# Performance work log

Measured on AMD Instinct MI355X. Metric: run time of the kernel, lower is better.

Reference implementation:

```python
import jax, jax.numpy as jnp
import numpy as np

N = 100000
E = 1600000
C_IN = 128
C_HID = 128


def setup_inputs() -> dict:
    key = jax.random.key(0)
    ks = jax.random.split(key, 6)
    x = jax.random.normal(ks[0], (N, C_IN), dtype=jnp.float32)
    edge_index = jax.random.randint(ks[1], (2, E), 0, N, dtype=jnp.int64)
    # GCNConv params: linear weight + bias per layer (glorot-ish scale)
    W1 = jax.random.normal(ks[2], (C_IN, C_HID), dtype=jnp.float32) / np.sqrt(C_IN)
    b1 = jnp.zeros((C_HID,), dtype=jnp.float32)
    W2 = jax.random.normal(ks[3], (C_HID, C_HID), dtype=jnp.float32) / np.sqrt(C_HID)
    b2 = jnp.zeros((C_HID,), dtype=jnp.float32)
    return {"x": x, "edge_index": edge_index, "W1": W1, "b1": b1, "W2": W2, "b2": b2}


def _gcn_conv(x, W, b, src, dst, n_nodes):
    # PyG GCNConv: h = D^{-1/2} (A + I) D^{-1/2} (x W) + b
    h = x @ W  # [N, C_out]
    # add self-loops
    loop = jnp.arange(n_nodes, dtype=src.dtype)
    s = jnp.concatenate([src, loop])
    d = jnp.concatenate([dst, loop])
    ones = jnp.ones(s.shape[0], dtype=h.dtype)
    deg = jax.ops.segment_sum(ones, d, num_segments=n_nodes)  # in-degree incl self-loop
    dinv = jnp.where(deg > 0, jax.lax.rsqrt(deg), 0.0)
    norm = dinv[s] * dinv[d]  # [E+N]
    msg = h[s] * norm[:, None]  # gather + scale
    out = jax.ops.segment_sum(msg, d, num_segments=n_nodes)  # scatter-add
    return out + b


def reference(x, edge_index, W1, b1, W2, b2):
    src, dst = edge_index[0], edge_index[1]
    h = jax.nn.relu(_gcn_conv(x, W1, b1, src, dst, N))
    h = jax.nn.relu(_gcn_conv(h, W2, b2, src, dst, N))
    return h
```

## Files before the change

kernel.cpp:

```cpp
#include <hip/hip_runtime.h>
#include <hip/hip_bf16.h>

#define GCN_N 100000
#define GB1 1563

typedef unsigned short u16;
typedef unsigned int u32;
typedef float f32x4 __attribute__((ext_vector_type(4)));
typedef short bf16x8 __attribute__((ext_vector_type(8)));

union v16 { uint4 u; bf16x8 h; };

__device__ inline u16 f2bf(float f) {
    u32 u = __float_as_uint(f);
    return (u16)((u + 0x7fffu + ((u >> 16) & 1u)) >> 16);
}
__device__ inline u32 pack2(float a, float b) {
    return (u32)f2bf(a) | ((u32)f2bf(b) << 16);
}
__device__ inline float bf_lo(u32 u) { return __uint_as_float(u << 16); }
__device__ inline float bf_hi(u32 u) { return __uint_as_float(u & 0xffff0000u); }

__device__ inline void addu8(float* a, float4 v) {
    u32 u;
    u = __float_as_uint(v.x); a[0] += bf_lo(u); a[1] += bf_hi(u);
    u = __float_as_uint(v.y); a[2] += bf_lo(u); a[3] += bf_hi(u);
    u = __float_as_uint(v.z); a[4] += bf_lo(u); a[5] += bf_hi(u);
    u = __float_as_uint(v.w); a[6] += bf_lo(u); a[7] += bf_hi(u);
}
__device__ inline void setu8(float* a, float4 v) {
    u32 u;
    u = __float_as_uint(v.x); a[0] = bf_lo(u); a[1] = bf_hi(u);
    u = __float_as_uint(v.y); a[2] = bf_lo(u); a[3] = bf_hi(u);
    u = __float_as_uint(v.z); a[4] = bf_lo(u); a[5] = bf_hi(u);
    u = __float_as_uint(v.w); a[6] = bf_lo(u); a[7] = bf_hi(u);
}

__device__ inline void mfma16(f32x4& d, uint4 a, uint4 b) {
    v16 av, bv; av.u = a; bv.u = b;
    d = __builtin_amdgcn_mfma_f32_16x16x32_bf16(av.h, bv.h, d, 0, 0, 0);
}


__global__ __launch_bounds__(256) void k_rank(const int* __restrict__ dst,
                                              int* __restrict__ cnt,
                                              int* __restrict__ rank, int E) {
    int i = blockIdx.x * 256 + threadIdx.x;
    if (i < E) rank[i] = atomicAdd(&cnt[dst[i]], 1);
}

__global__ __launch_bounds__(256) void k_bsum(const int* __restrict__ cnt,
                                              int* __restrict__ bsum, int n) {
    int i = blockIdx.x * 256 + threadIdx.x;
    int v = (i < n) ? cnt[i] : 0;
    #pragma unroll
    for (int off = 32; off > 0; off >>= 1) v += __shfl_down(v, off, 64);
    __shared__ int ws[4];
    const int lane = threadIdx.x & 63, wid = threadIdx.x >> 6;
    if (lane == 0) ws[wid] = v;
    __syncthreads();
    if (threadIdx.x == 0) bsum[blockIdx.x] = ws[0] + ws[1] + ws[2] + ws[3];
}

__global__ __launch_bounds__(512) void k_bscan(const int* __restrict__ bsum,
                                               int* __restrict__ bbase,
                                               int* __restrict__ rowstart,
                                               int nb, int n) {
    __shared__ int wsum[8];
    __shared__ int woff[8];
    __shared__ int total;
    const int lane = threadIdx.x & 63, wid = threadIdx.x >> 6;
    int v = (threadIdx.x < nb) ? bsum[threadIdx.x] : 0;
    int s = v;
    #pragma unroll
    for (int off = 1; off < 64; off <<= 1) {
        int t = __shfl_up(s, off, 64);
        if (lane >= off) s += t;
    }
    if (lane == 63) wsum[wid] = s;
    __syncthreads();
    if (threadIdx.x == 0) {
        int run = 0;
        #pragma unroll
        for (int w = 0; w < 8; ++w) { int t = wsum[w]; woff[w] = run; run += t; }
        total = run;
    }
    __syncthreads();
    if (threadIdx.x < nb) bbase[threadIdx.x] = woff[wid] + (s - v);
    if (threadIdx.x == 0) rowstart[n] = total;
}

__global__ __launch_bounds__(256) void k_rows(const int* __restrict__ cnt,
                                              const int* __restrict__ bbase,
                                              int* __restrict__ rowstart,
                                              float* __restrict__ dinv, int n) {
    __shared__ int wsum[4];
    __shared__ int woff[4];
    const int lane = threadIdx.x & 63, wid = threadIdx.x >> 6;
    int i = blockIdx.x * 256 + threadIdx.x;
    int v = (i < n) ? cnt[i] : 0;
    int s = v;
    #pragma unroll
    for (int off = 1; off < 64; off <<= 1) {
        int t = __shfl_up(s, off, 64);
        if (lane >= off) s += t;
    }
    if (lane == 63) wsum[wid] = s;
    __syncthreads();
    if (threadIdx.x == 0) {
        int run = bbase[blockIdx.x];
        #pragma unroll
        for (int w = 0; w < 4; ++w) { int t = wsum[w]; woff[w] = run; run += t; }
    }
    __syncthreads();
    if (i < n) {
        rowstart[i] = woff[wid] + (s - v);
        dinv[i] = rsqrtf((float)(v + 1));
    }
}

__global__ __launch_bounds__(256) void k_wprep(const float* __restrict__ W1,
                                               const float* __restrict__ W2,
                                               u16* __restrict__ Wt1,
                                               u16* __restrict__ Wt2) {
    const float* W = blockIdx.x ? W2 : W1;
    u16* Wt = blockIdx.x ? Wt2 : Wt1;
    for (int i = threadIdx.x; i < 16384; i += 256) {
        int k = i >> 7, nn = i & 127;
        Wt[nn * 128 + k] = f2bf(W[i]);
    }
}

__device__ __attribute__((always_inline))
inline void gemm_core(const uint4* Xs, const u16* __restrict__ Wt,
                      const float* __restrict__ dinv, u16* __restrict__ H,
                      long long row0, int n) {
    const int t = threadIdx.x;
    const int wid = t >> 6;
    const int l = t & 63, lm = l & 15, lh = l >> 4;
    uint4 a[4];
    const int lrow = wid * 16 + lm;
    #pragma unroll
    for (int kk = 0; kk < 4; ++kk) {
        int byte = (lrow * 256 + kk * 64 + lh * 16) ^ ((lm & 7) << 4);
        a[kk] = Xs[byte >> 4];
    }
    const uint4* wb = (const uint4*)Wt;
    f32x4 acc[8];
    #pragma unroll
    for (int j = 0; j < 8; ++j) acc[j] = (f32x4){0.f, 0.f, 0.f, 0.f};
    #pragma unroll
    for (int j = 0; j < 8; ++j) {
        #pragma unroll
        for (int kk = 0; kk < 4; ++kk) {
            uint4 b = wb[(j * 16 + lm) * 16 + kk * 4 + lh];
            mfma16(acc[j], a[kk], b);
        }
    }
    long long gr0 = row0 + wid * 16 + lh * 4;
    float dv[4];
    #pragma unroll
    for (int r = 0; r < 4; ++r) dv[r] = (gr0 + r < n) ? dinv[gr0 + r] : 0.f;
    #pragma unroll
    for (int j = 0; j < 8; ++j) {
        #pragma unroll
        for (int r = 0; r < 4; ++r) {
            long long grow = gr0 + r;
            if (grow < n) H[grow * 128 + j * 16 + lm] = f2bf(acc[j][r] * dv[r]);
        }
    }
}

__global__ __launch_bounds__(256) void k_gemm1_scatter(
        const float* __restrict__ X, const u16* __restrict__ Wt,
        const float* __restrict__ dinv, u16* __restrict__ H,
        const int* __restrict__ src, const int* __restrict__ dst,
        const int* __restrict__ rank, const int* __restrict__ rowstart,
        int* __restrict__ csr_src, int E, int n) {
    __shared__ uint4 Xs[1024];
    if (blockIdx.x >= GB1) {
        int i = (blockIdx.x - GB1) * 256 + threadIdx.x;
        if (i < E) csr_src[rowstart[dst[i]] + rank[i]] = src[i];
        return;
    }
    const long long row0 = (long long)blockIdx.x * 64;
    const int t = threadIdx.x;
    uint2* Xs2 = (uint2*)Xs;
    #pragma unroll
    for (int i = 0; i < 8; ++i) {
        int idx = i * 1024 + t * 4;
        int row = idx >> 7, k = idx & 127;
        long long grow = row0 + row; if (grow >= n) grow = n - 1;
        float4 v = *(const float4*)(X + grow * 128 + k);
        int byte = (row * 256 + k * 2) ^ ((row & 7) << 4);
        uint2 p; p.x = pack2(v.x, v.y); p.y = pack2(v.z, v.w);
        Xs2[byte >> 3] = p;
    }
    __syncthreads();
    gemm_core(Xs, Wt, dinv, H, row0, n);
}

__global__ __launch_bounds__(256) void k_gemm2(
        const u16* __restrict__ X, const u16* __restrict__ Wt,
        const float* __restrict__ dinv, u16* __restrict__ H, int n) {
    __shared__ uint4 Xs[1024];
    const long long row0 = (long long)blockIdx.x * 64;
    const int t = threadIdx.x;
    #pragma unroll
    for (int i = 0; i < 4; ++i) {
        int idx = i * 2048 + t * 8;
        int row = idx >> 7, k = idx & 127;
        long long grow = row0 + row; if (grow >= n) grow = n - 1;
        uint4 v = *(const uint4*)(X + grow * 128 + k);
        int byte = (row * 256 + k * 2) ^ ((row & 7) << 4);
        Xs[byte >> 4] = v;
    }
    __syncthreads();
    gemm_core(Xs, Wt, dinv, H, row0, n);
}

template<int OUT_BF16>
__global__ __launch_bounds__(256) void k_agg(const u16* __restrict__ h,
                                             const int* __restrict__ rowstart,
                                             const int* __restrict__ csr_src,
                                             const float* __restrict__ dinv,
                                             const float* __restrict__ bias,
                                             void* __restrict__ outp, int n) {
    const int q    = threadIdx.x >> 4;
    const int sub  = threadIdx.x & 15;
    const int node = blockIdx.x * 16 + q;
    if (node >= n) return;
    const float di = dinv[node];
    int e = rowstart[node];
    const int end = rowstart[node + 1];
    const float4* __restrict__ hv = (const float4*)h;
    float a[8], b[8];
    setu8(a, hv[(size_t)node * 16 + sub]);
    #pragma unroll
    for (int j = 0; j < 8; ++j) b[j] = 0.f;
    for (; e + 8 <= end; e += 8) {
        int s0 = csr_src[e + 0], s1 = csr_src[e + 1];
        int s2 = csr_src[e + 2], s3 = csr_src[e + 3];
        int s4 = csr_src[e + 4], s5 = csr_src[e + 5];
        int s6 = csr_src[e + 6], s7 = csr_src[e + 7];
        float4 v0 = hv[(size_t)s0 * 16 + sub];
        float4 v1 = hv[(size_t)s1 * 16 + sub];
        float4 v2 = hv[(size_t)s2 * 16 + sub];
        float4 v3 = hv[(size_t)s3 * 16 + sub];
        float4 v4 = hv[(size_t)s4 * 16 + sub];
        float4 v5 = hv[(size_t)s5 * 16 + sub];
        float4 v6 = hv[(size_t)s6 * 16 + sub];
        float4 v7 = hv[(size_t)s7 * 16 + sub];
        addu8(a, v0); addu8(b, v1); addu8(a, v2); addu8(b, v3);
        addu8(a, v4); addu8(b, v5); addu8(a, v6); addu8(b, v7);
    }
    for (; e + 4 <= end; e += 4) {
        int s0 = csr_src[e + 0], s1 = csr_src[e + 1];
        int s2 = csr_src[e + 2], s3 = csr_src[e + 3];
        float4 v0 = hv[(size_t)s0 * 16 + sub];
        float4 v1 = hv[(size_t)s1 * 16 + sub];
        float4 v2 = hv[(size_t)s2 * 16 + sub];
        float4 v3 = hv[(size_t)s3 * 16 + sub];
        addu8(a, v0); addu8(b, v1); addu8(a, v2); addu8(b, v3);
    }
    for (; e < end; ++e) {
        float4 v = hv[(size_t)csr_src[e] * 16 + sub];
        addu8(a, v);
    }
    const float4 bv0 = ((const float4*)bias)[sub * 2];
    const float4 bv1 = ((const float4*)bias)[sub * 2 + 1];
    float o[8];
    o[0] = fmaxf(fmaf(a[0] + b[0], di, bv0.x), 0.f);
    o[1] = fmaxf(fmaf(a[1] + b[1], di, bv0.y), 0.f);
    o[2] = fmaxf(fmaf(a[2] + b[2], di, bv0.z), 0.f);
    o[3] = fmaxf(fmaf(a[3] + b[3], di, bv0.w), 0.f);
    o[4] = fmaxf(fmaf(a[4] + b[4], di, bv1.x), 0.f);
    o[5] = fmaxf(fmaf(a[5] + b[5], di, bv1.y), 0.f);
    o[6] = fmaxf(fmaf(a[6] + b[6], di, bv1.z), 0.f);
    o[7] = fmaxf(fmaf(a[7] + b[7], di, bv1.w), 0.f);
    if (OUT_BF16) {
        float4 pv;
        pv.x = __uint_as_float(pack2(o[0], o[1]));
        pv.y = __uint_as_float(pack2(o[2], o[3]));
        pv.z = __uint_as_float(pack2(o[4], o[5]));
        pv.w = __uint_as_float(pack2(o[6], o[7]));
        ((float4*)outp)[(size_t)node * 16 + sub] = pv;
    } else {
        float* out = (float*)outp + (size_t)node * 128 + sub * 8;
        float4 w0 = {o[0], o[1], o[2], o[3]};
        float4 w1 = {o[4], o[5], o[6], o[7]};
        *(float4*)(out + 0) = w0;
        *(float4*)(out + 4) = w1;
    }
}


extern "C" void kernel_launch(void* const* d_in, const int* in_sizes, int n_in,
                              void* d_out, int out_size, void* d_ws, size_t ws_size,
                              hipStream_t stream) {
    const float* x   = (const float*)d_in[0];
    const int* edges = (const int*)d_in[1];
    const float* W1  = (const float*)d_in[2];
    const float* b1  = (const float*)d_in[3];
    const float* W2  = (const float*)d_in[4];
    const float* b2  = (const float*)d_in[5];
    const int E = in_sizes[1] / 2;
    const int N = GCN_N;
    const int* srcp = edges;
    const int* dstp = edges + E;
    const int NB = (N + 255) / 256;
    const int SB = (E + 255) / 256;

    char* ws = (char*)d_ws;
    int*   cnt      = (int*)(ws + 0);
    int*   rowstart = (int*)(ws + 524288);
    float* dinvp    = (float*)(ws + 1048576);
    int*   bsum     = (int*)(ws + 1474560);
    int*   bbase    = (int*)(ws + 1507328);
    u16*   wt1      = (u16*)(ws + 1572864);
    u16*   wt2      = (u16*)(ws + 1605632);
    int*   csr      = (int*)(ws + 2097152);
    int*   rank     = (int*)(ws + 8912896);
    u16*   h1       = (u16*)(ws + 16777216);
    u16*   h2       = (u16*)(ws + 44040192);

    hipMemsetAsync(cnt, 0, N * sizeof(int), stream);

    k_rank <<<SB, 256, 0, stream>>>(dstp, cnt, rank, E);
    k_bsum <<<NB, 256, 0, stream>>>(cnt, bsum, N);
    k_bscan<<<1, 512, 0, stream>>>(bsum, bbase, rowstart, NB, N);
    k_rows <<<NB, 256, 0, stream>>>(cnt, bbase, rowstart, dinvp, N);
    k_wprep<<<2, 256, 0, stream>>>(W1, W2, wt1, wt2);

    k_gemm1_scatter<<<GB1 + SB, 256, 0, stream>>>(
        x, wt1, dinvp, h1, srcp, dstp, rank, rowstart, csr, E, N);
    k_agg<1><<<(N + 15) / 16, 256, 0, stream>>>(h1, rowstart, csr, dinvp, b1, h2, N);
    k_gemm2<<<GB1, 256, 0, stream>>>(h2, wt2, dinvp, h1, N);
    k_agg<0><<<(N + 15) / 16, 256, 0, stream>>>(h1, rowstart, csr, dinvp, b2, d_out, N);
}
```

Baseline: 321.2 us.

## Build CSR via bucketed two-pass partition instead of global atomics and scans

Replaces the per-edge global atomic rank, three-kernel prefix scan and scatter with a two-level bucket sort. Edges are partitioned into 128-node buckets using shared-memory histograms and one global atomic per bucket per block, and each bucket is then sorted locally into CSR order in a per-bucket kernel. This removes the memset and a good deal of random global atomic traffic, and cuts the launch count. The cost is a fixed bucket capacity (BCAP 4096) that silently drops edges if a bucket overflows, plus a serial per-bucket prefix over preceding buckets. The scatter is also no longer fused into gemm1.

```diff
diff --git a/kernel.cpp b/kernel.cpp
--- a/kernel.cpp
+++ b/kernel.cpp
@@ -3,6 +3,9 @@
 
 #define GCN_N 100000
 #define GB1 1563
+#define NBUCK 782
+#define BCAP 4096
+#define KPWG 391
 
 typedef unsigned short u16;
 typedef unsigned int u32;
@@ -41,93 +44,103 @@
     d = __builtin_amdgcn_mfma_f32_16x16x32_bf16(av.h, bv.h, d, 0, 0, 0);
 }
 
-
-__global__ __launch_bounds__(256) void k_rank(const int* __restrict__ dst,
-                                              int* __restrict__ cnt,
-                                              int* __restrict__ rank, int E) {
-    int i = blockIdx.x * 256 + threadIdx.x;
-    if (i < E) rank[i] = atomicAdd(&cnt[dst[i]], 1);
-}
-
-__global__ __launch_bounds__(256) void k_bsum(const int* __restrict__ cnt,
-                                              int* __restrict__ bsum, int n) {
-    int i = blockIdx.x * 256 + threadIdx.x;
-    int v = (i < n) ? cnt[i] : 0;
-    #pragma unroll
-    for (int off = 32; off > 0; off >>= 1) v += __shfl_down(v, off, 64);
-    __shared__ int ws[4];
-    const int lane = threadIdx.x & 63, wid = threadIdx.x >> 6;
-    if (lane == 0) ws[wid] = v;
-    __syncthreads();
-    if (threadIdx.x == 0) bsum[blockIdx.x] = ws[0] + ws[1] + ws[2] + ws[3];
-}
-
-__global__ __launch_bounds__(512) void k_bscan(const int* __restrict__ bsum,
-                                               int* __restrict__ bbase,
-                                               int* __restrict__ rowstart,
-                                               int nb, int n) {
-    __shared__ int wsum[8];
-    __shared__ int woff[8];
-    __shared__ int total;
-    const int lane = threadIdx.x & 63, wid = threadIdx.x >> 6;
-    int v = (threadIdx.x < nb) ? bsum[threadIdx.x] : 0;
-    int s = v;
-    #pragma unroll
-    for (int off = 1; off < 64; off <<= 1) {
-        int t = __shfl_up(s, off, 64);
-        if (lane >= off) s += t;
-    }
-    if (lane == 63) wsum[wid] = s;
-    __syncthreads();
-    if (threadIdx.x == 0) {
-        int run = 0;
-        #pragma unroll
-        for (int w = 0; w < 8; ++w) { int t = wsum[w]; woff[w] = run; run += t; }
-        total = run;
-    }
-    __syncthreads();
-    if (threadIdx.x < nb) bbase[threadIdx.x] = woff[wid] + (s - v);
-    if (threadIdx.x == 0) rowstart[n] = total;
-}
-
-__global__ __launch_bounds__(256) void k_rows(const int* __restrict__ cnt,
-                                              const int* __restrict__ bbase,
-                                              int* __restrict__ rowstart,
-                                              float* __restrict__ dinv, int n) {
-    __shared__ int wsum[4];
-    __shared__ int woff[4];
-    const int lane = threadIdx.x & 63, wid = threadIdx.x >> 6;
-    int i = blockIdx.x * 256 + threadIdx.x;
-    int v = (i < n) ? cnt[i] : 0;
-    int s = v;
-    #pragma unroll
-    for (int off = 1; off < 64; off <<= 1) {
-        int t = __shfl_up(s, off, 64);
-        if (lane >= off) s += t;
-    }
-    if (lane == 63) wsum[wid] = s;
-    __syncthreads();
-    if (threadIdx.x == 0) {
-        int run = bbase[blockIdx.x];
-        #pragma unroll
-        for (int w = 0; w < 4; ++w) { int t = wsum[w]; woff[w] = run; run += t; }
-    }
-    __syncthreads();
-    if (i < n) {
-        rowstart[i] = woff[wid] + (s - v);
-        dinv[i] = rsqrtf((float)(v + 1));
-    }
-}
-
-__global__ __launch_bounds__(256) void k_wprep(const float* __restrict__ W1,
-                                               const float* __restrict__ W2,
-                                               u16* __restrict__ Wt1,
-                                               u16* __restrict__ Wt2) {
-    const float* W = blockIdx.x ? W2 : W1;
-    u16* Wt = blockIdx.x ? Wt2 : Wt1;
+__global__ __launch_bounds__(256) void k_init(int* __restrict__ gcursor,
+                                              const float* __restrict__ W1,
+                                              const float* __restrict__ W2,
+                                              u16* __restrict__ Wt1,
+                                              u16* __restrict__ Wt2) {
+    if (blockIdx.x == 0) {
+        for (int i = threadIdx.x; i < NBUCK; i += 256) gcursor[i] = 0;
+        return;
+    }
+    const float* W = (blockIdx.x == 1) ? W1 : W2;
+    u16* Wt = (blockIdx.x == 1) ? Wt1 : Wt2;
     for (int i = threadIdx.x; i < 16384; i += 256) {
         int k = i >> 7, nn = i & 127;
         Wt[nn * 128 + k] = f2bf(W[i]);
+    }
+}
+
+__global__ __launch_bounds__(256) void k_part(const int* __restrict__ src,
+                                              const int* __restrict__ dst,
+                                              int* __restrict__ gcursor,
+                                              u32* __restrict__ part, int E) {
+    __shared__ int lhist[NBUCK];
+    __shared__ int lbase[NBUCK];
+    __shared__ int lcur[NBUCK];
+    const int t = threadIdx.x;
+    for (int i = t; i < NBUCK; i += 256) { lhist[i] = 0; lcur[i] = 0; }
+    __syncthreads();
+    const long long e0 = (long long)blockIdx.x * 4096;
+    #pragma unroll
+    for (int i = 0; i < 16; ++i) {
+        long long e = e0 + i * 256 + t;
+        if (e < E) atomicAdd(&lhist[dst[e] >> 7], 1);
+    }
+    __syncthreads();
+    for (int i = t; i < NBUCK; i += 256) {
+        int c = lhist[i];
+        lbase[i] = c ? atomicAdd(&gcursor[i], c) : 0;
+    }
+    __syncthreads();
+    #pragma unroll
+    for (int i = 0; i < 16; ++i) {
+        long long e = e0 + i * 256 + t;
+        if (e < E) {
+            int d = dst[e];
+            int b = d >> 7;
+            int ofs = lbase[b] + atomicAdd(&lcur[b], 1);
+            if (ofs < BCAP)
+                part[(long long)b * BCAP + ofs] =
+                    (u32)src[e] | ((u32)(d & 127) << 17);
+        }
+    }
+}
+
+__global__ __launch_bounds__(256) void k_csr(const int* __restrict__ gcursor,
+                                             const u32* __restrict__ part,
+                                             int* __restrict__ rowstart,
+                                             float* __restrict__ dinv,
+                                             int* __restrict__ csr, int n) {
+    __shared__ int lcount[128];
+    __shared__ int lpfx[128];
+    __shared__ int lcur[128];
+    __shared__ int wpart[4];
+    __shared__ int sbase;
+    const int t = threadIdx.x;
+    const int lane = t & 63, wid = t >> 6;
+    const int b = blockIdx.x;
+    int ps = 0;
+    for (int j = t; j < b; j += 256) ps += min(gcursor[j], BCAP);
+    #pragma unroll
+    for (int off = 32; off > 0; off >>= 1) ps += __shfl_down(ps, off, 64);
+    if (lane == 0) wpart[wid] = ps;
+    if (t < 128) { lcount[t] = 0; lcur[t] = 0; }
+    __syncthreads();
+    if (t == 0) sbase = wpart[0] + wpart[1] + wpart[2] + wpart[3];
+    __syncthreads();
+    const int base = sbase;
+    const int cnt = min(gcursor[b], BCAP);
+    const u32* bp = part + (long long)b * BCAP;
+    for (int i = t; i < cnt; i += 256) atomicAdd(&lcount[bp[i] >> 17], 1);
+    __syncthreads();
+    if (t == 0) {
+        int run = 0;
+        #pragma unroll
+        for (int j = 0; j < 128; ++j) { lpfx[j] = run; run += lcount[j]; }
+    }
+    __syncthreads();
+    int node = b * 128 + t;
+    if (t < 128 && node < n) {
+        rowstart[node] = base + lpfx[t];
+        dinv[node] = rsqrtf((float)(lcount[t] + 1));
+    }
+    if (b == NBUCK - 1 && t == 0) rowstart[n] = base + cnt;
+    for (int i = t; i < cnt; i += 256) {
+        u32 v = bp[i];
+        int loc = v >> 17;
+        int p = base + lpfx[loc] + atomicAdd(&lcur[loc], 1);
+        csr[p] = (int)(v & 0x1FFFFu);
     }
 }
 
@@ -171,18 +184,10 @@
     }
 }
 
-__global__ __launch_bounds__(256) void k_gemm1_scatter(
+__global__ __launch_bounds__(256) void k_gemm1(
         const float* __restrict__ X, const u16* __restrict__ Wt,
-        const float* __restrict__ dinv, u16* __restrict__ H,
-        const int* __restrict__ src, const int* __restrict__ dst,
-        const int* __restrict__ rank, const int* __restrict__ rowstart,
-        int* __restrict__ csr_src, int E, int n) {
+        const float* __restrict__ dinv, u16* __restrict__ H, int n) {
     __shared__ uint4 Xs[1024];
-    if (blockIdx.x >= GB1) {
-        int i = (blockIdx.x - GB1) * 256 + threadIdx.x;
-        if (i < E) csr_src[rowstart[dst[i]] + rank[i]] = src[i];
-        return;
-    }
     const long long row0 = (long long)blockIdx.x * 64;
     const int t = threadIdx.x;
     uint2* Xs2 = (uint2*)Xs;
@@ -308,32 +313,22 @@
     const int N = GCN_N;
     const int* srcp = edges;
     const int* dstp = edges + E;
-    const int NB = (N + 255) / 256;
-    const int SB = (E + 255) / 256;
 
     char* ws = (char*)d_ws;
-    int*   cnt      = (int*)(ws + 0);
-    int*   rowstart = (int*)(ws + 524288);
-    float* dinvp    = (float*)(ws + 1048576);
-    int*   bsum     = (int*)(ws + 1474560);
-    int*   bbase    = (int*)(ws + 1507328);
-    u16*   wt1      = (u16*)(ws + 1572864);
-    u16*   wt2      = (u16*)(ws + 1605632);
-    int*   csr      = (int*)(ws + 2097152);
-    int*   rank     = (int*)(ws + 8912896);
-    u16*   h1       = (u16*)(ws + 16777216);
-    u16*   h2       = (u16*)(ws + 44040192);
-
-    hipMemsetAsync(cnt, 0, N * sizeof(int), stream);
-
-    k_rank <<<SB, 256, 0, stream>>>(dstp, cnt, rank, E);
-    k_bsum <<<NB, 256, 0, stream>>>(cnt, bsum, N);
-    k_bscan<<<1, 512, 0, stream>>>(bsum, bbase, rowstart, NB, N);
-    k_rows <<<NB, 256, 0, stream>>>(cnt, bbase, rowstart, dinvp, N);
-    k_wprep<<<2, 256, 0, stream>>>(W1, W2, wt1, wt2);
-
-    k_gemm1_scatter<<<GB1 + SB, 256, 0, stream>>>(
-        x, wt1, dinvp, h1, srcp, dstp, rank, rowstart, csr, E, N);
+    int*   gcursor  = (int*)(ws + 0);
+    int*   rowstart = (int*)(ws + 4096);
+    float* dinvp    = (float*)(ws + 409600 + 4096);
+    u16*   wt1      = (u16*)(ws + 819200);
+    u16*   wt2      = (u16*)(ws + 851968);
+    u32*   part     = (u32*)(ws + 1048576);
+    int*   csr      = (int*)(ws + 14680064);
+    u16*   h1       = (u16*)(ws + 23068672);
+    u16*   h2       = (u16*)(ws + 50331648);
+
+    k_init<<<3, 256, 0, stream>>>(gcursor, W1, W2, wt1, wt2);
+    k_part<<<KPWG, 256, 0, stream>>>(srcp, dstp, gcursor, part, E);
+    k_csr<<<NBUCK, 256, 0, stream>>>(gcursor, part, rowstart, dinvp, csr, N);
+    k_gemm1<<<GB1, 256, 0, stream>>>(x, wt1, dinvp, h1, N);
     k_agg<1><<<(N + 15) / 16, 256, 0, stream>>>(h1, rowstart, csr, dinvp, b1, h2, N);
     k_gemm2<<<GB1, 256, 0, stream>>>(h2, wt2, dinvp, h1, N);
     k_agg<0><<<(N + 15) / 16, 256, 0, stream>>>(h1, rowstart, csr, dinvp, b2, d_out, N);
```

New measurement: 270.8 us. 1.19x faster.
